# Performance work log

Measured on AMD Instinct MI355X. Metric: run time of the kernel, lower is better.

Reference implementation:

```python
import jax, jax.numpy as jnp
import numpy as np

B, C, D, H, W = 2, 64, 20, 20, 20
RATIO = 8
CQ = C // RATIO  # Q/K channels = 8


def setup_inputs() -> dict:
    key = jax.random.key(0)
    ks = jax.random.split(key, 8)
    s = 0.05
    return {
        "x": jax.random.normal(ks[0], (B, C, D, H, W), dtype=jnp.float32),
        "Wq": jax.random.normal(ks[1], (CQ, C), dtype=jnp.float32) * s,
        "bq": jax.random.normal(ks[2], (CQ,), dtype=jnp.float32) * s,
        "Wk": jax.random.normal(ks[3], (CQ, C), dtype=jnp.float32) * s,
        "bk": jax.random.normal(ks[4], (CQ,), dtype=jnp.float32) * s,
        "Wv": jax.random.normal(ks[5], (C, C), dtype=jnp.float32) * s,
        "bv": jax.random.normal(ks[6], (C,), dtype=jnp.float32) * s,
        "gamma": jax.random.normal(ks[7], (1,), dtype=jnp.float32) * s,
    }


def reference(x, Wq, bq, Wk, bk, Wv, bv, gamma):
    b, c, *spatial = x.shape
    n = int(np.prod(spatial))
    xf = x.reshape(b, c, n)  # [B, C, N]
    # 1x1 convs == per-position channel matmuls
    Q = jnp.einsum('oc,bcn->bon', Wq, xf) + bq[None, :, None]  # [B, Cq, N]
    K = jnp.einsum('oc,bcn->bon', Wk, xf) + bk[None, :, None]  # [B, Cq, N]
    V = jnp.einsum('oc,bcn->bon', Wv, xf) + bv[None, :, None]  # [B, C, N]
    # energy[b, n, m] = sum_q Q[b, q, n] * K[b, q, m]  (no scaling, as in source)
    energy = jnp.einsum('bqn,bqm->bnm', Q, K)  # [B, N, N]
    attention = jax.nn.softmax(energy, axis=-1)
    # out[b, c, n] = sum_m V[b, c, m] * attention[b, n, m]
    out = jnp.einsum('bcm,bnm->bcn', V, attention)
    out = out.reshape(b, c, *spatial)
    return gamma * out + x
```

## Files before the change

kernel.cpp:

```cpp
#include <hip/hip_runtime.h>
#include <hip/hip_bf16.h>

#define BB 2
#define CC 64
#define CQk 8
#define NN 8000
#define QT 4
#define NWAVE 8
#define NBLK32 250

using f32x4  = __attribute__((ext_vector_type(4))) float;
using bf16x8 = __attribute__((ext_vector_type(8))) short;
typedef unsigned short ushort_t;
typedef unsigned int uint_t;

__device__ __forceinline__ ushort_t f2bf(float f) {
    __hip_bfloat16 h = __float2bfloat16(f);
    return *reinterpret_cast<ushort_t*>(&h);
}

__device__ __forceinline__ float exp2_fast(float x) {
#if __has_builtin(__builtin_amdgcn_exp2f)
    return __builtin_amdgcn_exp2f(x);
#else
    return exp2f(x);
#endif
}

__device__ __forceinline__ uint_t pack_bf16(float a, float b) {
    const uint_t ua = __builtin_bit_cast(uint_t, a) + 0x8000u;
    const uint_t ub = __builtin_bit_cast(uint_t, b) + 0x8000u;
    return (ua >> 16) | (ub & 0xFFFF0000u);
}

__global__ void detect_dtype(const void* __restrict__ x, int* __restrict__ flag)
{
    const float* xf = (const float*)x;
    const int t = threadIdx.x;
    const float a = fabsf(xf[t * 8]);
    const int ok = (a > 9.765625e-4f && a < 16.0f) ? 1 : 0;
    const unsigned long long m = __ballot(ok);
    if (t == 0) flag[0] = (__popcll(m) >= 48) ? 1 : 0;
}

__device__ __forceinline__ float loadF(const void* p, size_t i, int isf) {
    return isf ? ((const float*)p)[i]
               : __bfloat162float(((const __hip_bfloat16*)p)[i]);
}

__device__ __forceinline__ int vidx(int n) {
    const int h = (n & 15) >> 2;
    const int i = (n & 3) + (((n >> 4) & 1) << 2);
    return (n & ~31) + h * 8 + i;
}

__global__ __launch_bounds__(320) void qkv_kernel(
    const void* __restrict__ x,
    const void* __restrict__ Wq, const void* __restrict__ bq,
    const void* __restrict__ Wk, const void* __restrict__ bk,
    const void* __restrict__ Wv, const void* __restrict__ bv,
    ushort_t* __restrict__ Qbf, ushort_t* __restrict__ Kbf,
    ushort_t* __restrict__ Vtp, const int* __restrict__ flag)
{
    __shared__ float sW[80][CC];
    __shared__ float sB[80];
    __shared__ float sX[CC][64];
    const int isf = flag[0];
    const int t = threadIdx.x;

    for (int i = t; i < 80 * CC; i += 320) {
        const int r = i >> 6, c = i & 63;
        float w;
        if (r < CQk)          w = loadF(Wq, (size_t)r * CC + c, isf);
        else if (r < 2 * CQk) w = loadF(Wk, (size_t)(r - CQk) * CC + c, isf);
        else                  w = loadF(Wv, (size_t)(r - 2 * CQk) * CC + c, isf);
        sW[r][c] = w;
    }
    if (t < 80) {
        float bias;
        if (t < CQk)          bias = loadF(bq, t, isf);
        else if (t < 2 * CQk) bias = loadF(bk, t - CQk, isf);
        else                  bias = loadF(bv, t - 2 * CQk, isf);
        sB[t] = bias;
    }
    const int blk = blockIdx.x;
    const int b = blk / 125;
    const int n0 = (blk % 125) * 64;
    for (int i = t; i < CC * 64; i += 320) {
        const int c = i >> 6, nl = i & 63;
        sX[c][nl] = loadF(x, (size_t)b * CC * NN + (size_t)c * NN + n0 + nl, isf);
    }
    __syncthreads();

    const int rg = t >> 6;
    const int nl = t & 63;
    const int n = n0 + nl;
    const int r0 = rg * 16;

    float xv[CC];
#pragma unroll
    for (int c = 0; c < CC; ++c) xv[c] = sX[c][nl];

    float acc[16];
#pragma unroll
    for (int rr = 0; rr < 16; ++rr) {
        const f32x4* w4 = (const f32x4*)&sW[r0 + rr][0];
        float a0 = 0.f, a1 = 0.f, a2 = 0.f, a3 = 0.f;
#pragma unroll
        for (int c4 = 0; c4 < 16; ++c4) {
            const f32x4 wv = w4[c4];
            a0 += wv.x * xv[c4 * 4 + 0];
            a1 += wv.y * xv[c4 * 4 + 1];
            a2 += wv.z * xv[c4 * 4 + 2];
            a3 += wv.w * xv[c4 * 4 + 3];
        }
        acc[rr] = sB[r0 + rr] + ((a0 + a1) + (a2 + a3));
    }

    const size_t pn = (size_t)b * NN + n;
    if (rg == 0) {
        bf16x8 pq, pk, z8;
#pragma unroll
        for (int j = 0; j < 8; ++j) {
            pq[j] = (short)f2bf(acc[j] * 1.44269504089f);
            pk[j] = (short)f2bf(acc[8 + j]);
            z8[j] = 0;
        }
        *(bf16x8*)&Qbf[pn * 8] = pq;
        *(bf16x8*)&Kbf[pn * 32]      = pk;
        *(bf16x8*)&Kbf[pn * 32 + 8]  = z8;
        *(bf16x8*)&Kbf[pn * 32 + 16] = z8;
        *(bf16x8*)&Kbf[pn * 32 + 24] = z8;
    } else {
        const int c0 = (rg - 1) * 16;
        const int vn = vidx(n);
#pragma unroll
        for (int rr = 0; rr < 16; ++rr)
            Vtp[((size_t)b * CC + c0 + rr) * NN + vn] = f2bf(acc[rr]);
    }
}

#define KSTEP (16 * 32 * 32)
#define VSTEP (16 * 32)

#define LOADK(d0, d1, ko) do { \
    d0 = *(const bf16x8*)(Kb + (ko)); \
    d1 = *(const bf16x8*)(Kb + (ko) + 512); } while (0)

#define LOADV(v0, v1, v2, v3, vo) do { \
    v0 = *(const bf16x8*)(Vb + (vo)); \
    v1 = *(const bf16x8*)(Vb + 16 * NN + (vo)); \
    v2 = *(const bf16x8*)(Vb + 32 * NN + (vo)); \
    v3 = *(const bf16x8*)(Vb + 48 * NN + (vo)); } while (0)

#define MKAF(af, eA, eB) do { \
    union { uint_t u[4]; bf16x8 v; } _u; \
    _u.u[0] = pack_bf16(exp2_fast(eA[0]), exp2_fast(eA[1])); \
    _u.u[1] = pack_bf16(exp2_fast(eA[2]), exp2_fast(eA[3])); \
    _u.u[2] = pack_bf16(exp2_fast(eB[0]), exp2_fast(eB[1])); \
    _u.u[3] = pack_bf16(exp2_fast(eB[2]), exp2_fast(eB[3])); \
    af = _u.v; } while (0)

#define COMPUTE(ka0, ka1, v0, v1, v2, v3) do { \
    f32x4 e00 = __builtin_amdgcn_mfma_f32_16x16x32_bf16(ka0, qb[0], zf, 0, 0, 0); \
    f32x4 e10 = __builtin_amdgcn_mfma_f32_16x16x32_bf16(ka1, qb[0], zf, 0, 0, 0); \
    f32x4 e01 = __builtin_amdgcn_mfma_f32_16x16x32_bf16(ka0, qb[1], zf, 0, 0, 0); \
    f32x4 e11 = __builtin_amdgcn_mfma_f32_16x16x32_bf16(ka1, qb[1], zf, 0, 0, 0); \
    f32x4 e02 = __builtin_amdgcn_mfma_f32_16x16x32_bf16(ka0, qb[2], zf, 0, 0, 0); \
    f32x4 e12 = __builtin_amdgcn_mfma_f32_16x16x32_bf16(ka1, qb[2], zf, 0, 0, 0); \
    f32x4 e03 = __builtin_amdgcn_mfma_f32_16x16x32_bf16(ka0, qb[3], zf, 0, 0, 0); \
    f32x4 e13 = __builtin_amdgcn_mfma_f32_16x16x32_bf16(ka1, qb[3], zf, 0, 0, 0); \
    bf16x8 af0, af1, af2, af3; \
    MKAF(af0, e00, e10); MKAF(af1, e01, e11); \
    MKAF(af2, e02, e12); MKAF(af3, e03, e13); \
    acc[0][0] = __builtin_amdgcn_mfma_f32_16x16x32_bf16(af0, v0, acc[0][0], 0, 0, 0); \
    acc[0][1] = __builtin_amdgcn_mfma_f32_16x16x32_bf16(af0, v1, acc[0][1], 0, 0, 0); \
    acc[0][2] = __builtin_amdgcn_mfma_f32_16x16x32_bf16(af0, v2, acc[0][2], 0, 0, 0); \
    acc[0][3] = __builtin_amdgcn_mfma_f32_16x16x32_bf16(af0, v3, acc[0][3], 0, 0, 0); \
    lac[0]    = __builtin_amdgcn_mfma_f32_16x16x32_bf16(af0, ones, lac[0], 0, 0, 0); \
    acc[1][0] = __builtin_amdgcn_mfma_f32_16x16x32_bf16(af1, v0, acc[1][0], 0, 0, 0); \
    acc[1][1] = __builtin_amdgcn_mfma_f32_16x16x32_bf16(af1, v1, acc[1][1], 0, 0, 0); \
    acc[1][2] = __builtin_amdgcn_mfma_f32_16x16x32_bf16(af1, v2, acc[1][2], 0, 0, 0); \
    acc[1][3] = __builtin_amdgcn_mfma_f32_16x16x32_bf16(af1, v3, acc[1][3], 0, 0, 0); \
    lac[1]    = __builtin_amdgcn_mfma_f32_16x16x32_bf16(af1, ones, lac[1], 0, 0, 0); \
    acc[2][0] = __builtin_amdgcn_mfma_f32_16x16x32_bf16(af2, v0, acc[2][0], 0, 0, 0); \
    acc[2][1] = __builtin_amdgcn_mfma_f32_16x16x32_bf16(af2, v1, acc[2][1], 0, 0, 0); \
    acc[2][2] = __builtin_amdgcn_mfma_f32_16x16x32_bf16(af2, v2, acc[2][2], 0, 0, 0); \
    acc[2][3] = __builtin_amdgcn_mfma_f32_16x16x32_bf16(af2, v3, acc[2][3], 0, 0, 0); \
    lac[2]    = __builtin_amdgcn_mfma_f32_16x16x32_bf16(af2, ones, lac[2], 0, 0, 0); \
    acc[3][0] = __builtin_amdgcn_mfma_f32_16x16x32_bf16(af3, v0, acc[3][0], 0, 0, 0); \
    acc[3][1] = __builtin_amdgcn_mfma_f32_16x16x32_bf16(af3, v1, acc[3][1], 0, 0, 0); \
    acc[3][2] = __builtin_amdgcn_mfma_f32_16x16x32_bf16(af3, v2, acc[3][2], 0, 0, 0); \
    acc[3][3] = __builtin_amdgcn_mfma_f32_16x16x32_bf16(af3, v3, acc[3][3], 0, 0, 0); \
    lac[3]    = __builtin_amdgcn_mfma_f32_16x16x32_bf16(af3, ones, lac[3], 0, 0, 0); \
} while (0)

__global__ __launch_bounds__(512, 2) void attn_fused(
    const ushort_t* __restrict__ Qbf, const ushort_t* __restrict__ Kbf,
    const ushort_t* __restrict__ Vtp,
    const void* __restrict__ x, const void* __restrict__ gamma,
    void* __restrict__ out, const int* __restrict__ flag)
{
    __shared__ float sO[64][65];
    __shared__ float sL[64];
    const int isf = flag[0];
    const int tid = threadIdx.x;
    const int lane = tid & 63;
    const int w = tid >> 6;
    const int cl = lane & 15, h = lane >> 4;
    const int q0 = blockIdx.x * 64;
    const int b = blockIdx.y;
    const size_t bN = (size_t)b * NN;

    for (int i = tid; i < 64 * 65; i += 512) (&sO[0][0])[i] = 0.f;
    if (tid < 64) sL[tid] = 0.f;
    __syncthreads();

    bf16x8 zero8;
#pragma unroll
    for (int j = 0; j < 8; ++j) zero8[j] = 0;
    bf16x8 qb[QT];
#pragma unroll
    for (int t = 0; t < QT; ++t) {
        bf16x8 z = zero8;
        if (h == 0) z = *(const bf16x8*)&Qbf[(bN + q0 + t * 16 + cl) * 8];
        qb[t] = z;
    }
    bf16x8 ones;
#pragma unroll
    for (int j = 0; j < 8; ++j) ones[j] = (short)0x3F80;

    const f32x4 zf = {0.f, 0.f, 0.f, 0.f};
    f32x4 acc[QT][4];
    f32x4 lac[QT];
#pragma unroll
    for (int t = 0; t < QT; ++t) {
        lac[t] = zf;
#pragma unroll
        for (int ct = 0; ct < 4; ++ct) acc[t][ct] = zf;
    }

    const ushort_t* Kb = Kbf + bN * 32;
    const ushort_t* Vb = Vtp + (size_t)b * CC * NN;

    uint_t koA = (uint_t)(w * 32 + cl) * 32 + h * 8;
    uint_t voA = (uint_t)cl * NN + w * 32 + h * 8;
    uint_t koB = koA + 8 * 32 * 32;
    uint_t voB = voA + 8 * 32;
    int baA = w, baB = w + 8;

    bf16x8 ka0A, ka1A, vA0, vA1, vA2, vA3;
    bf16x8 ka0B, ka1B, vB0, vB1, vB2, vB3;

    LOADK(ka0A, ka1A, koA); LOADV(vA0, vA1, vA2, vA3, voA);
    baA += 16; if (baA < NBLK32) { koA += KSTEP; voA += VSTEP; }

    const int cnt = (w < 2) ? 32 : 31;
    const int pairs = cnt >> 1;
    for (int p = 0; p < pairs; ++p) {
        LOADK(ka0B, ka1B, koB); LOADV(vB0, vB1, vB2, vB3, voB);
        baB += 16; if (baB < NBLK32) { koB += KSTEP; voB += VSTEP; }
        COMPUTE(ka0A, ka1A, vA0, vA1, vA2, vA3);
        LOADK(ka0A, ka1A, koA); LOADV(vA0, vA1, vA2, vA3, voA);
        baA += 16; if (baA < NBLK32) { koA += KSTEP; voA += VSTEP; }
        COMPUTE(ka0B, ka1B, vB0, vB1, vB2, vB3);
    }
    if (cnt & 1) COMPUTE(ka0A, ka1A, vA0, vA1, vA2, vA3);

#pragma unroll
    for (int t = 0; t < QT; ++t) {
#pragma unroll
        for (int ct = 0; ct < 4; ++ct)
#pragma unroll
            for (int r = 0; r < 4; ++r)
                atomicAdd(&sO[t * 16 + 4 * h + r][ct * 16 + cl], acc[t][ct][r]);
        if (cl == 0) {
#pragma unroll
            for (int r = 0; r < 4; ++r)
                atomicAdd(&sL[t * 16 + 4 * h + r], lac[t][r]);
        }
    }
    __syncthreads();

    const float g = loadF(gamma, 0, isf);
    const int qq = tid & 63;
    const int crow = tid >> 6;
    const float rL = 1.0f / sL[qq];
#pragma unroll
    for (int p = 0; p < 8; ++p) {
        const int c = p * 8 + crow;
        const size_t idx = ((size_t)b * CC + c) * NN + q0 + qq;
        if (isf) {
            const float xr = __builtin_nontemporal_load((const float*)x + idx);
            __builtin_nontemporal_store(g * sO[qq][c] * rL + xr, (float*)out + idx);
        } else {
            const float xr = __bfloat162float(((const __hip_bfloat16*)x)[idx]);
            ((__hip_bfloat16*)out)[idx] = __float2bfloat16(g * sO[qq][c] * rL + xr);
        }
    }
}

extern "C" void kernel_launch(void* const* d_in, const int* in_sizes, int n_in,
                              void* d_out, int out_size, void* d_ws, size_t ws_size,
                              hipStream_t stream)
{
    const void* x     = d_in[0];
    const void* Wq    = d_in[1];
    const void* bq    = d_in[2];
    const void* Wk    = d_in[3];
    const void* bk    = d_in[4];
    const void* Wv    = d_in[5];
    const void* bv    = d_in[6];
    const void* gamma = d_in[7];

    char* base = (char*)d_ws;
    int* flag = (int*)base;
    size_t off = 256;
    ushort_t* Qbf = (ushort_t*)(base + off); off += (size_t)BB * NN * CQk * 2;
    ushort_t* Kbf = (ushort_t*)(base + off); off += (size_t)BB * NN * 32 * 2;
    ushort_t* Vtp = (ushort_t*)(base + off); off += ((size_t)BB * CC * NN + 64) * 2;

    detect_dtype<<<1, 64, 0, stream>>>(x, flag);

    qkv_kernel<<<dim3(250), 320, 0, stream>>>(x, Wq, bq, Wk, bk, Wv, bv,
                                              Qbf, Kbf, Vtp, flag);

    dim3 g2(NN / 64, BB);
    attn_fused<<<g2, 512, 0, stream>>>(Qbf, Kbf, Vtp, x, gamma, d_out, flag);
}
```

Before: 106.7 us.

## Store K and V in MFMA fragment order for contiguous per-wave loads

The QKV projection kernel now writes K and V directly in the per-lane MFMA fragment layout. Each wave in the attention kernel then loads one contiguous 1 KB chunk per fragment instead of strided rows separated by NN. The projection kernel also doubles its threads to 640, with each row group computing 8 outputs instead of 16, to spread the work. The cost is more scattered 2-byte stores for V in the projection kernel and tight coupling between the two kernels' index maths.

```diff
diff --git a/kernel.cpp b/kernel.cpp
--- a/kernel.cpp
+++ b/kernel.cpp
@@ -48,19 +48,13 @@
                : __bfloat162float(((const __hip_bfloat16*)p)[i]);
 }
 
-__device__ __forceinline__ int vidx(int n) {
-    const int h = (n & 15) >> 2;
-    const int i = (n & 3) + (((n >> 4) & 1) << 2);
-    return (n & ~31) + h * 8 + i;
-}
-
-__global__ __launch_bounds__(320) void qkv_kernel(
+__global__ __launch_bounds__(640) void qkv_kernel(
     const void* __restrict__ x,
     const void* __restrict__ Wq, const void* __restrict__ bq,
     const void* __restrict__ Wk, const void* __restrict__ bk,
     const void* __restrict__ Wv, const void* __restrict__ bv,
-    ushort_t* __restrict__ Qbf, ushort_t* __restrict__ Kbf,
-    ushort_t* __restrict__ Vtp, const int* __restrict__ flag)
+    ushort_t* __restrict__ Qbf, ushort_t* __restrict__ Kfrag,
+    ushort_t* __restrict__ Vfrag, const int* __restrict__ flag)
 {
     __shared__ float sW[80][CC];
     __shared__ float sB[80];
@@ -68,7 +62,7 @@
     const int isf = flag[0];
     const int t = threadIdx.x;
 
-    for (int i = t; i < 80 * CC; i += 320) {
+    for (int i = t; i < 80 * CC; i += 640) {
         const int r = i >> 6, c = i & 63;
         float w;
         if (r < CQk)          w = loadF(Wq, (size_t)r * CC + c, isf);
@@ -86,7 +80,7 @@
     const int blk = blockIdx.x;
     const int b = blk / 125;
     const int n0 = (blk % 125) * 64;
-    for (int i = t; i < CC * 64; i += 320) {
+    for (int i = t; i < CC * 64; i += 640) {
         const int c = i >> 6, nl = i & 63;
         sX[c][nl] = loadF(x, (size_t)b * CC * NN + (size_t)c * NN + n0 + nl, isf);
     }
@@ -95,15 +89,15 @@
     const int rg = t >> 6;
     const int nl = t & 63;
     const int n = n0 + nl;
-    const int r0 = rg * 16;
+    const int r0 = rg * 8;
 
     float xv[CC];
 #pragma unroll
     for (int c = 0; c < CC; ++c) xv[c] = sX[c][nl];
 
-    float acc[16];
-#pragma unroll
-    for (int rr = 0; rr < 16; ++rr) {
+    float acc[8];
+#pragma unroll
+    for (int rr = 0; rr < 8; ++rr) {
         const f32x4* w4 = (const f32x4*)&sW[r0 + rr][0];
         float a0 = 0.f, a1 = 0.f, a2 = 0.f, a3 = 0.f;
 #pragma unroll
@@ -117,31 +111,39 @@
         acc[rr] = sB[r0 + rr] + ((a0 + a1) + (a2 + a3));
     }
 
-    const size_t pn = (size_t)b * NN + n;
+    const int mblk = n >> 5;
     if (rg == 0) {
-        bf16x8 pq, pk, z8;
-#pragma unroll
-        for (int j = 0; j < 8; ++j) {
-            pq[j] = (short)f2bf(acc[j] * 1.44269504089f);
-            pk[j] = (short)f2bf(acc[8 + j]);
-            z8[j] = 0;
+        bf16x8 pq;
+#pragma unroll
+        for (int j = 0; j < 8; ++j) pq[j] = (short)f2bf(acc[j] * 1.44269504089f);
+        *(bf16x8*)&Qbf[((size_t)b * NN + n) * 8] = pq;
+    } else if (rg == 1) {
+        bf16x8 pk, z8;
+#pragma unroll
+        for (int j = 0; j < 8; ++j) { pk[j] = (short)f2bf(acc[j]); z8[j] = 0; }
+        const int rloc = n & 31, jj = rloc >> 4, cl16 = rloc & 15;
+        ushort_t* kb = Kfrag + (size_t)b * NN * 32
+                     + ((size_t)(mblk * 2 + jj) * 64) * 8;
+        *(bf16x8*)&kb[(cl16) * 8]      = pk;
+        *(bf16x8*)&kb[(16 + cl16) * 8] = z8;
+        *(bf16x8*)&kb[(32 + cl16) * 8] = z8;
+        *(bf16x8*)&kb[(48 + cl16) * 8] = z8;
+    } else {
+        const int c0 = (rg - 2) * 8;
+        const int hv = (n & 15) >> 2;
+        const int iv = (n & 3) + (((n >> 4) & 1) << 2);
+        ushort_t* vb = Vfrag + (size_t)b * NN * 64;
+#pragma unroll
+        for (int rr = 0; rr < 8; ++rr) {
+            const int c = c0 + rr;
+            vb[((size_t)(mblk * 4 + (c >> 4)) * 64 + hv * 16 + (c & 15)) * 8 + iv]
+                = f2bf(acc[rr]);
         }
-        *(bf16x8*)&Qbf[pn * 8] = pq;
-        *(bf16x8*)&Kbf[pn * 32]      = pk;
-        *(bf16x8*)&Kbf[pn * 32 + 8]  = z8;
-        *(bf16x8*)&Kbf[pn * 32 + 16] = z8;
-        *(bf16x8*)&Kbf[pn * 32 + 24] = z8;
-    } else {
-        const int c0 = (rg - 1) * 16;
-        const int vn = vidx(n);
-#pragma unroll
-        for (int rr = 0; rr < 16; ++rr)
-            Vtp[((size_t)b * CC + c0 + rr) * NN + vn] = f2bf(acc[rr]);
-    }
-}
-
-#define KSTEP (16 * 32 * 32)
-#define VSTEP (16 * 32)
+    }
+}
+
+#define KSTEP (16 * 1024)
+#define VSTEP (16 * 2048)
 
 #define LOADK(d0, d1, ko) do { \
     d0 = *(const bf16x8*)(Kb + (ko)); \
@@ -149,9 +151,9 @@
 
 #define LOADV(v0, v1, v2, v3, vo) do { \
     v0 = *(const bf16x8*)(Vb + (vo)); \
-    v1 = *(const bf16x8*)(Vb + 16 * NN + (vo)); \
-    v2 = *(const bf16x8*)(Vb + 32 * NN + (vo)); \
-    v3 = *(const bf16x8*)(Vb + 48 * NN + (vo)); } while (0)
+    v1 = *(const bf16x8*)(Vb + (vo) + 512); \
+    v2 = *(const bf16x8*)(Vb + (vo) + 1024); \
+    v3 = *(const bf16x8*)(Vb + (vo) + 1536); } while (0)
 
 #define MKAF(af, eA, eB) do { \
     union { uint_t u[4]; bf16x8 v; } _u; \
@@ -196,8 +198,8 @@
 } while (0)
 
 __global__ __launch_bounds__(512, 2) void attn_fused(
-    const ushort_t* __restrict__ Qbf, const ushort_t* __restrict__ Kbf,
-    const ushort_t* __restrict__ Vtp,
+    const ushort_t* __restrict__ Qbf, const ushort_t* __restrict__ Kfrag,
+    const ushort_t* __restrict__ Vfrag,
     const void* __restrict__ x, const void* __restrict__ gamma,
     void* __restrict__ out, const int* __restrict__ flag)
 {
@@ -240,13 +242,13 @@
         for (int ct = 0; ct < 4; ++ct) acc[t][ct] = zf;
     }
 
-    const ushort_t* Kb = Kbf + bN * 32;
-    const ushort_t* Vb = Vtp + (size_t)b * CC * NN;
-
-    uint_t koA = (uint_t)(w * 32 + cl) * 32 + h * 8;
-    uint_t voA = (uint_t)cl * NN + w * 32 + h * 8;
-    uint_t koB = koA + 8 * 32 * 32;
-    uint_t voB = voA + 8 * 32;
+    const ushort_t* Kb = Kfrag + bN * 32;
+    const ushort_t* Vb = Vfrag + bN * 64;
+
+    uint_t koA = (uint_t)w * 1024 + lane * 8;
+    uint_t voA = (uint_t)w * 2048 + lane * 8;
+    uint_t koB = koA + 8 * 1024;
+    uint_t voB = voA + 8 * 2048;
     int baA = w, baB = w + 8;
 
     bf16x8 ka0A, ka1A, vA0, vA1, vA2, vA3;
@@ -316,15 +318,15 @@
     char* base = (char*)d_ws;
     int* flag = (int*)base;
     size_t off = 256;
-    ushort_t* Qbf = (ushort_t*)(base + off); off += (size_t)BB * NN * CQk * 2;
-    ushort_t* Kbf = (ushort_t*)(base + off); off += (size_t)BB * NN * 32 * 2;
-    ushort_t* Vtp = (ushort_t*)(base + off); off += ((size_t)BB * CC * NN + 64) * 2;
+    ushort_t* Qbf   = (ushort_t*)(base + off); off += (size_t)BB * NN * CQk * 2;
+    ushort_t* Kfrag = (ushort_t*)(base + off); off += (size_t)BB * NN * 32 * 2;
+    ushort_t* Vfrag = (ushort_t*)(base + off); off += (size_t)BB * NN * 64 * 2;
 
     detect_dtype<<<1, 64, 0, stream>>>(x, flag);
 
-    qkv_kernel<<<dim3(250), 320, 0, stream>>>(x, Wq, bq, Wk, bk, Wv, bv,
-                                              Qbf, Kbf, Vtp, flag);
+    qkv_kernel<<<dim3(250), 640, 0, stream>>>(x, Wq, bq, Wk, bk, Wv, bv,
+                                              Qbf, Kfrag, Vfrag, flag);
 
     dim3 g2(NN / 64, BB);
-    attn_fused<<<g2, 512, 0, stream>>>(Qbf, Kbf, Vtp, x, gamma, d_out, flag);
-}
+    attn_fused<<<g2, 512, 0, stream>>>(Qbf, Kfrag, Vfrag, x, gamma, d_out, flag);
+}
```

Result: slower. 128.0 us (+20.0%).
